# Optimization experiments

Hardware: AMD Instinct MI355X
Metric: run time of the kernel (lower is better)

Reference implementation:

```python
import jax, jax.numpy as jnp
import numpy as np

HIDDEN = 512
HEADS = 8
HEAD_DIM = HIDDEN // HEADS
THRESH = 0.1
EPS = 1e-8


def setup_inputs() -> dict:
    key = jax.random.key(0)
    ks = jax.random.split(key, 9)
    B, S = 2, 4096
    scale = 1.0 / np.sqrt(HIDDEN)
    x = jax.random.normal(ks[0], (B, S, HIDDEN), dtype=jnp.float32)
    Wq = jax.random.normal(ks[1], (HIDDEN, HIDDEN), dtype=jnp.float32) * scale
    bq = jnp.zeros((HIDDEN,), dtype=jnp.float32)
    Wk = jax.random.normal(ks[2], (HIDDEN, HIDDEN), dtype=jnp.float32) * scale
    bk = jnp.zeros((HIDDEN,), dtype=jnp.float32)
    Wv = jax.random.normal(ks[3], (HIDDEN, HIDDEN), dtype=jnp.float32) * scale
    bv = jnp.zeros((HIDDEN,), dtype=jnp.float32)
    Wo = jax.random.normal(ks[4], (HIDDEN, HIDDEN), dtype=jnp.float32) * scale
    bo = jnp.zeros((HIDDEN,), dtype=jnp.float32)
    return {"x": x, "Wq": Wq, "bq": bq, "Wk": Wk, "bk": bk,
            "Wv": Wv, "bv": bv, "Wo": Wo, "bo": bo}


def reference(x, Wq, bq, Wk, bk, Wv, bv, Wo, bo):
    B, S, _ = x.shape
    # torch Linear: y = x @ W.T + b
    def proj(W, b):
        y = jnp.einsum('bsd,ed->bse', x, W) + b
        return y.reshape(B, S, HEADS, HEAD_DIM).transpose(0, 2, 1, 3)  # [B,H,S,Dh]
    Q = proj(Wq, bq)
    K = proj(Wk, bk)
    V = proj(Wv, bv)
    scores = jnp.einsum('bhqd,bhkd->bhqk', Q, K) / jnp.sqrt(jnp.float32(HEAD_DIM))
    probs = jax.nn.softmax(scores, axis=-1)  # [B,H,S,S]
    probs = jnp.where(probs > THRESH, probs, 0.0)
    probs = probs / (jnp.sum(probs, axis=-1, keepdims=True) + EPS)
    ctx = jnp.einsum('bhqk,bhkd->bhqd', probs, V)
    ctx = ctx.transpose(0, 2, 1, 3).reshape(B, S, HIDDEN)
    return jnp.einsum('bsd,ed->bse', ctx, Wo) + bo
```

## Files before the change

kernel.cpp:

```cpp
#include <hip/hip_runtime.h>

#define S_LEN 4096
#define BATCH 2
#define HID 512
#define HEADS 8
#define HD 64
#define NX (BATCH * S_LEN * HID)
#define WSZ (HID * HID)
#define NBH (BATCH * HEADS)
#define QB 32
#define NB1 (S_LEN / QB * NBH)
#define NB2 (S_LEN / 64 * NBH)

typedef short v8s __attribute__((ext_vector_type(8)));
typedef float v4f __attribute__((ext_vector_type(4)));
typedef float v16f __attribute__((ext_vector_type(16)));
typedef unsigned short ushort_t;
typedef const __attribute__((address_space(1))) unsigned gu32;
typedef __attribute__((address_space(3))) unsigned lu32;

__device__ __forceinline__ ushort_t f2bf(float f) {
  unsigned u = __builtin_bit_cast(unsigned, f);
  u += 0x7fffu + ((u >> 16) & 1u);
  return (ushort_t)(u >> 16);
}
__device__ __forceinline__ unsigned pk2(float a, float b) {
  return (__builtin_bit_cast(unsigned, a) >> 16) |
         (__builtin_bit_cast(unsigned, b) & 0xFFFF0000u);
}
__device__ __forceinline__ float fexp2(float x) {
  return __builtin_amdgcn_exp2f(x);
}


__global__ __launch_bounds__(256) void cvt_k(
    const float* __restrict__ x,
    const float* __restrict__ wq, const float* __restrict__ wk,
    const float* __restrict__ wv, const float* __restrict__ wo,
    ushort_t* __restrict__ dst)
{
  const size_t e = ((size_t)blockIdx.x * 256 + threadIdx.x) * 4;
  const float* src; size_t off;
  if (e < NX) { src = x; off = e; }
  else {
    const size_t we = e - NX;
    const int wi = (int)(we >> 18);
    src = wi == 0 ? wq : wi == 1 ? wk : wi == 2 ? wv : wo;
    off = we & (WSZ - 1);
  }
  float4 v = *(const float4*)&src[off];
  uint2 u; u.x = pk2(v.x, v.y); u.y = pk2(v.z, v.w);
  *(uint2*)&dst[e] = u;
}

__global__ __launch_bounds__(256) void gemm_qkv(
    const ushort_t* __restrict__ X, const ushort_t* __restrict__ Wb,
    const float* __restrict__ bq, const float* __restrict__ bk, const float* __restrict__ bv,
    ushort_t* __restrict__ Qf, ushort_t* __restrict__ Kf, ushort_t* __restrict__ Vw,
    float qscale)
{
  __shared__ ushort_t As[128][32];
  __shared__ ushort_t Bs[128][32];
  const int t = threadIdx.x;
  const int lane = t & 63;
  const int l15 = lane & 15, lg = lane >> 4;
  const int w = t >> 6;
  const int wr = w >> 1, wc = w & 1;
  const int m0 = blockIdx.y * 128;
  const int wsel = blockIdx.x >> 2;
  const int e0 = (blockIdx.x & 3) * 128;
  const ushort_t* W = Wb + (size_t)wsel * WSZ;
  const float* bias = wsel == 0 ? bq : wsel == 1 ? bk : bv;
  const float osc = (wsel == 0) ? qscale : 1.0f;

  v4f acc[4][4] = {};
  const int r0 = t >> 2, c0 = (t & 3) * 8;

  for (int k0 = 0; k0 < HID; k0 += 32) {
    __syncthreads();
    __builtin_amdgcn_global_load_lds(
        (gu32*)(const void*)&X[(size_t)(m0 + r0) * HID + k0 + c0],
        (lu32*)(void*)&As[r0][c0], 16, 0, 0);
    __builtin_amdgcn_global_load_lds(
        (gu32*)(const void*)&X[(size_t)(m0 + r0 + 64) * HID + k0 + c0],
        (lu32*)(void*)&As[r0 + 64][c0], 16, 0, 0);
    __builtin_amdgcn_global_load_lds(
        (gu32*)(const void*)&W[(size_t)(e0 + r0) * HID + k0 + c0],
        (lu32*)(void*)&Bs[r0][c0], 16, 0, 0);
    __builtin_amdgcn_global_load_lds(
        (gu32*)(const void*)&W[(size_t)(e0 + r0 + 64) * HID + k0 + c0],
        (lu32*)(void*)&Bs[r0 + 64][c0], 16, 0, 0);
    __syncthreads();
    v8s a[4], b[4];
    #pragma unroll
    for (int fr = 0; fr < 4; ++fr)
      a[fr] = *(const v8s*)&As[wr * 64 + 16 * fr + l15][8 * lg];
    #pragma unroll
    for (int fc = 0; fc < 4; ++fc)
      b[fc] = *(const v8s*)&Bs[wc * 64 + 16 * fc + l15][8 * lg];
    #pragma unroll
    for (int fr = 0; fr < 4; ++fr)
      #pragma unroll
      for (int fc = 0; fc < 4; ++fc)
        acc[fr][fc] = __builtin_amdgcn_mfma_f32_16x16x32_bf16(a[fr], b[fc], acc[fr][fc], 0, 0, 0);
  }

  #pragma unroll
  for (int fr = 0; fr < 4; ++fr)
    #pragma unroll
    for (int fc = 0; fc < 4; ++fc) {
      const int e = e0 + wc * 64 + 16 * fc + l15;
      const float bval = bias[e];
      #pragma unroll
      for (int r = 0; r < 4; ++r) {
        const int m = m0 + wr * 64 + 16 * fr + 4 * lg + r;
        const float v = (acc[fr][fc][r] + bval) * osc;
        const int bidx = m >> 12, s = m & (S_LEN - 1);
        const int hh = e >> 6, dh = e & 63;
        const size_t hb = ((size_t)(bidx * HEADS + hh)) * (size_t)(S_LEN * HD);
        if (wsel == 2) {
          Vw[hb + (size_t)s * HD + dh] = f2bf(v);
        } else {
          const size_t off = (size_t)(s >> 5) * 2048 +
              (size_t)(((dh >> 4) * 64 + ((dh >> 3) & 1) * 32 + (s & 31)) * 8 + (dh & 7));
          (wsel == 0 ? Qf : Kf)[hb + off] = f2bf(v);
        }
      }
    }
}

__global__ __launch_bounds__(256, 4) void attn_p1(
    const ushort_t* __restrict__ Qf, const ushort_t* __restrict__ Kf,
    int* __restrict__ Flg)
{
  __shared__ float RedL[4][QB];
  __shared__ float RedM[4][QB];
  __shared__ int bflag;
  const int t = threadIdx.x;
  const int lane = t & 63;
  const int l31 = lane & 31, hi = lane >> 5;
  const int kq = t >> 6;
  const int lin = blockIdx.x;
  const int bh = ((lin & 7) << 1) | ((lin >> 3) & 1);
  const int q0 = (lin >> 4) * QB;
  if (t == 0) bflag = 0;

  const size_t hoff = (size_t)bh * (size_t)(S_LEN * HD);
  const ushort_t* Qb = Qf + hoff + (size_t)(q0 >> 5) * 2048;
  const ushort_t* Kb = Kf + hoff;

  v8s qa[4];
  #pragma unroll
  for (int ks = 0; ks < 4; ++ks)
    qa[ks] = *(const v8s*)&Qb[(ks * 64 + lane) * 8];

  float M[16], L[16];
  #pragma unroll
  for (int j = 0; j < 16; ++j) { M[j] = -1e30f; L[j] = 0.f; }

  v8s kA[4], kB4[4];
  {
    const ushort_t* kc = Kb + (size_t)kq * 2048;
    #pragma unroll
    for (int ks = 0; ks < 4; ++ks)
      kA[ks] = *(const v8s*)&kc[(ks * 64 + lane) * 8];
  }

#define PROC(KX)                                                            \
  {                                                                         \
    v16f s = {};                                                            \
    _Pragma("unroll")                                                       \
    for (int ks = 0; ks < 4; ++ks)                                          \
      s = __builtin_amdgcn_mfma_f32_32x32x16_bf16(qa[ks], KX[ks], s, 0, 0, 0); \
    _Pragma("unroll")                                                       \
    for (int j = 0; j < 16; ++j) {                                          \
      M[j] = fmaxf(M[j], s[j]);                                             \
      L[j] += fexp2(s[j]);                                                  \
    }                                                                       \
  }

  for (int i = 0; i < 32; i += 2) {
    {
      const ushort_t* kc = Kb + (size_t)(kq + 4 * (i + 1)) * 2048;
      #pragma unroll
      for (int ks = 0; ks < 4; ++ks)
        kB4[ks] = *(const v8s*)&kc[(ks * 64 + lane) * 8];
    }
    PROC(kA)
    {
      const int c2 = (i + 2 < 32) ? (kq + 4 * (i + 2)) : kq;
      const ushort_t* kc = Kb + (size_t)c2 * 2048;
      #pragma unroll
      for (int ks = 0; ks < 4; ++ks)
        kA[ks] = *(const v8s*)&kc[(ks * 64 + lane) * 8];
    }
    PROC(kB4)
  }
#undef PROC

  #pragma unroll
  for (int j = 0; j < 16; ++j) {
    float Lv = L[j], Mv = M[j];
    Lv += __shfl_xor(Lv, 1);  Mv = fmaxf(Mv, __shfl_xor(Mv, 1));
    Lv += __shfl_xor(Lv, 2);  Mv = fmaxf(Mv, __shfl_xor(Mv, 2));
    Lv += __shfl_xor(Lv, 4);  Mv = fmaxf(Mv, __shfl_xor(Mv, 4));
    Lv += __shfl_xor(Lv, 8);  Mv = fmaxf(Mv, __shfl_xor(Mv, 8));
    Lv += __shfl_xor(Lv, 16); Mv = fmaxf(Mv, __shfl_xor(Mv, 16));
    if (l31 == 0) {
      const int row = (j & 3) + 8 * (j >> 2) + 4 * hi;
      RedL[kq][row] = Lv;
      RedM[kq][row] = Mv;
    }
  }
  __syncthreads();
  if (t < QB) {
    const float Lv = RedL[0][t] + RedL[1][t] + RedL[2][t] + RedL[3][t];
    const float Mv = fmaxf(fmaxf(RedM[0][t], RedM[1][t]),
                           fmaxf(RedM[2][t], RedM[3][t]));
    if (Mv >= __log2f(Lv) - 3.3719281f) atomicOr(&bflag, 1);
  }
  __syncthreads();
  if (t == 0) Flg[lin] = bflag;
}

__global__ __launch_bounds__(256) void attn_p2(
    const ushort_t* __restrict__ Qf, const ushort_t* __restrict__ Kf,
    const ushort_t* __restrict__ V, ushort_t* __restrict__ Cb,
    const int* __restrict__ Flg)
{
  const int lin = blockIdx.x;
  {
    const int base = lin & 15, qb = lin >> 4;
    if ((Flg[base | ((2 * qb) << 4)] | Flg[base | ((2 * qb + 1) << 4)]) == 0)
      return;
  }
  __shared__ float Osh[64][HD + 1];
  __shared__ float Dsh[64];
  __shared__ float RedA[4][64];
  __shared__ float iLs[64];
  __shared__ ushort_t Pp[4][32][40];
  __shared__ ushort_t VT[4][HD][40];
  const int t = threadIdx.x;
  const int lane = t & 63;
  const int l31 = lane & 31, hi = lane >> 5;
  const int w = t >> 6;
  const int bh = ((lin & 7) << 1) | ((lin >> 3) & 1);
  const int q0 = (lin >> 4) * 64;
  const size_t hoff = (size_t)bh * (size_t)(S_LEN * HD);
  const ushort_t* Qb = Qf + hoff + (size_t)(q0 >> 5) * 2048;
  const ushort_t* Kb = Kf + hoff;
  const ushort_t* Vh = V + hoff;

  if (t < 64) Dsh[t] = 0.f;
  for (int idx = t; idx < 64 * HD; idx += 256) Osh[idx >> 6][idx & 63] = 0.f;

  v8s qa[4], qB[4];
  #pragma unroll
  for (int ks = 0; ks < 4; ++ks) {
    qa[ks] = *(const v8s*)&Qb[(ks * 64 + lane) * 8];
    qB[ks] = *(const v8s*)&Qb[2048 + (ks * 64 + lane) * 8];
  }

  float L0[16], L1[16];
  #pragma unroll
  for (int j = 0; j < 16; ++j) { L0[j] = 0.f; L1[j] = 0.f; }
  for (int i = 0; i < 32; ++i) {
    const ushort_t* kc = Kb + (size_t)(w + 4 * i) * 2048;
    v8s kb[4];
    #pragma unroll
    for (int ks = 0; ks < 4; ++ks)
      kb[ks] = *(const v8s*)&kc[(ks * 64 + lane) * 8];
    v16f sa = {}, sb = {};
    #pragma unroll
    for (int ks = 0; ks < 4; ++ks) {
      sa = __builtin_amdgcn_mfma_f32_32x32x16_bf16(qa[ks], kb[ks], sa, 0, 0, 0);
      sb = __builtin_amdgcn_mfma_f32_32x32x16_bf16(qB[ks], kb[ks], sb, 0, 0, 0);
    }
    #pragma unroll
    for (int j = 0; j < 16; ++j) {
      L0[j] += fexp2(sa[j]);
      L1[j] += fexp2(sb[j]);
    }
  }
  #pragma unroll
  for (int rseti = 0; rseti < 2; ++rseti)
    #pragma unroll
    for (int j = 0; j < 16; ++j) {
      float Lv = (rseti == 0) ? L0[j] : L1[j];
      Lv += __shfl_xor(Lv, 1);  Lv += __shfl_xor(Lv, 2);
      Lv += __shfl_xor(Lv, 4);  Lv += __shfl_xor(Lv, 8);
      Lv += __shfl_xor(Lv, 16);
      if (l31 == 0) {
        const int row = rseti * 32 + (j & 3) + 8 * (j >> 2) + 4 * hi;
        RedA[w][row] = Lv;
      }
    }
  __syncthreads();
  if (t < 64)
    iLs[t] = 1.0f / (RedA[0][t] + RedA[1][t] + RedA[2][t] + RedA[3][t]);
  __syncthreads();

  float il[2][16];
  #pragma unroll
  for (int rseti = 0; rseti < 2; ++rseti)
    #pragma unroll
    for (int j = 0; j < 16; ++j)
      il[rseti][j] = iLs[rseti * 32 + (j & 3) + 8 * (j >> 2) + 4 * hi];

  v16f oA[2] = {}, oB[2] = {};
  float den[2][16] = {};

  for (int i = 0; i < 32; ++i) {
    const int c = w + 4 * i;
    const ushort_t* kc = Kb + (size_t)c * 2048;
    v8s kb[4];
    #pragma unroll
    for (int ks = 0; ks < 4; ++ks)
      kb[ks] = *(const v8s*)&kc[(ks * 64 + lane) * 8];
    v16f sa = {}, sb = {};
    #pragma unroll
    for (int ks = 0; ks < 4; ++ks) {
      sa = __builtin_amdgcn_mfma_f32_32x32x16_bf16(qa[ks], kb[ks], sa, 0, 0, 0);
      sb = __builtin_amdgcn_mfma_f32_32x32x16_bf16(qB[ks], kb[ks], sb, 0, 0, 0);
    }
    {
      const ushort_t* vsrc = &Vh[((size_t)c * 32 + l31) * HD + hi * 32];
      #pragma unroll
      for (int qq = 0; qq < 4; ++qq) {
        uint4 vv = *(const uint4*)&vsrc[qq * 8];
        const ushort_t* pv = (const ushort_t*)&vv;
        #pragma unroll
        for (int jj = 0; jj < 8; ++jj)
          VT[w][hi * 32 + qq * 8 + jj][l31] = pv[jj];
      }
    }
    #pragma unroll
    for (int rseti = 0; rseti < 2; ++rseti) {
      #pragma unroll
      for (int j = 0; j < 16; ++j) {
        const float s = (rseti == 0) ? sa[j] : sb[j];
        const int row = (j & 3) + 8 * (j >> 2) + 4 * hi;
        float p = fexp2(s) * il[rseti][j];
        p = (p > 0.1f) ? p : 0.f;
        den[rseti][j] += p;
        Pp[w][row][l31] = f2bf(p);
      }
      v8s pa0 = *(const v8s*)&Pp[w][l31][8 * hi];
      v8s pa1 = *(const v8s*)&Pp[w][l31][16 + 8 * hi];
      #pragma unroll
      for (int dblk = 0; dblk < 2; ++dblk) {
        v8s vb0 = *(const v8s*)&VT[w][dblk * 32 + l31][8 * hi];
        v8s vb1 = *(const v8s*)&VT[w][dblk * 32 + l31][16 + 8 * hi];
        if (rseti == 0) {
          oA[dblk] = __builtin_amdgcn_mfma_f32_32x32x16_bf16(pa0, vb0, oA[dblk], 0, 0, 0);
          oA[dblk] = __builtin_amdgcn_mfma_f32_32x32x16_bf16(pa1, vb1, oA[dblk], 0, 0, 0);
        } else {
          oB[dblk] = __builtin_amdgcn_mfma_f32_32x32x16_bf16(pa0, vb0, oB[dblk], 0, 0, 0);
          oB[dblk] = __builtin_amdgcn_mfma_f32_32x32x16_bf16(pa1, vb1, oB[dblk], 0, 0, 0);
        }
      }
    }
  }

  #pragma unroll
  for (int rseti = 0; rseti < 2; ++rseti)
    #pragma unroll
    for (int j = 0; j < 16; ++j) {
      float d = den[rseti][j];
      d += __shfl_xor(d, 1); d += __shfl_xor(d, 2); d += __shfl_xor(d, 4);
      d += __shfl_xor(d, 8); d += __shfl_xor(d, 16);
      const int row = rseti * 32 + (j & 3) + 8 * (j >> 2) + 4 * hi;
      if (l31 == 0) atomicAdd(&Dsh[row], d);
    }
  #pragma unroll
  for (int rseti = 0; rseti < 2; ++rseti)
    #pragma unroll
    for (int dblk = 0; dblk < 2; ++dblk)
      #pragma unroll
      for (int j = 0; j < 16; ++j) {
        const int row = rseti * 32 + (j & 3) + 8 * (j >> 2) + 4 * hi;
        const float val = (rseti == 0) ? oA[dblk][j] : oB[dblk][j];
        atomicAdd(&Osh[row][dblk * 32 + l31], val);
      }
  __syncthreads();
  const int b = bh >> 3, h = bh & 7;
  for (int idx = t; idx < 64 * HD; idx += 256) {
    const int row = idx >> 6, d = idx & 63;
    const float val = Osh[row][d] / (Dsh[row] + 1e-8f);
    Cb[((size_t)b * S_LEN + q0 + row) * HID + h * HD + d] = f2bf(val);
  }
}

__global__ __launch_bounds__(256) void gemm_out(
    const ushort_t* __restrict__ X, const ushort_t* __restrict__ W,
    const float* __restrict__ bias, const int* __restrict__ Flg,
    float* __restrict__ Df)
{
  const int t = threadIdx.x;
  const int m0 = blockIdx.y * 64;
  const int e0 = blockIdx.x * 64;

  int fm = 0;
  {
    const int b = m0 >> 12, qblk = (m0 & (S_LEN - 1)) >> 6;
    #pragma unroll
    for (int h = 0; h < HEADS; ++h) {
      const int bhh = b * HEADS + h;
      const int base = (bhh >> 1) | ((bhh & 1) << 3);
      const int f = Flg[base | ((2 * qblk) << 4)] |
                    Flg[base | ((2 * qblk + 1) << 4)];
      fm |= (f ? 1 : 0) << h;
    }
    if (!fm) {
      const int row = t >> 2, c0 = (t & 3) * 16;
      #pragma unroll
      for (int g = 0; g < 4; ++g) {
        const float4 bv = *(const float4*)&bias[e0 + c0 + g * 4];
        *(float4*)&Df[(size_t)(m0 + row) * HID + e0 + c0 + g * 4] = bv;
      }
      return;
    }
  }

  __shared__ ushort_t As[64][40];
  __shared__ ushort_t Bs[64][40];
  const int lane = t & 63;
  const int l15 = lane & 15, lg = lane >> 4;
  const int w = t >> 6;
  const int wr = w >> 1, wc = w & 1;

  v4f acc[2][2] = {};
  const int srow = t >> 2, scol = (t & 3) * 8;
  const uint4 zu = {0u, 0u, 0u, 0u};

  for (int k0 = 0; k0 < HID; k0 += 32) {
    __syncthreads();
    const bool hot = (fm >> (k0 >> 6)) & 1;
    *(uint4*)&As[srow][scol] = hot
        ? *(const uint4*)&X[(size_t)(m0 + srow) * HID + k0 + scol]
        : zu;
    *(uint4*)&Bs[srow][scol] =
        *(const uint4*)&W[(size_t)(e0 + srow) * HID + k0 + scol];
    __syncthreads();
    v8s a[2], b[2];
    #pragma unroll
    for (int fr = 0; fr < 2; ++fr)
      a[fr] = *(const v8s*)&As[wr * 32 + 16 * fr + l15][8 * lg];
    #pragma unroll
    for (int fc = 0; fc < 2; ++fc)
      b[fc] = *(const v8s*)&Bs[wc * 32 + 16 * fc + l15][8 * lg];
    #pragma unroll
    for (int fr = 0; fr < 2; ++fr)
      #pragma unroll
      for (int fc = 0; fc < 2; ++fc)
        acc[fr][fc] = __builtin_amdgcn_mfma_f32_16x16x32_bf16(a[fr], b[fc], acc[fr][fc], 0, 0, 0);
  }

  #pragma unroll
  for (int fr = 0; fr < 2; ++fr)
    #pragma unroll
    for (int fc = 0; fc < 2; ++fc) {
      const int e = e0 + wc * 32 + 16 * fc + l15;
      const float bval = bias[e];
      #pragma unroll
      for (int r = 0; r < 4; ++r) {
        const int m = m0 + wr * 32 + 16 * fr + 4 * lg + r;
        Df[(size_t)m * HID + e] = acc[fr][fc][r] + bval;
      }
    }
}

extern "C" void kernel_launch(void* const* d_in, const int* in_sizes, int n_in,
                              void* d_out, int out_size, void* d_ws, size_t ws_size,
                              hipStream_t stream) {
  const float* x  = (const float*)d_in[0];
  const float* Wq = (const float*)d_in[1];
  const float* bq = (const float*)d_in[2];
  const float* Wk = (const float*)d_in[3];
  const float* bk = (const float*)d_in[4];
  const float* Wv = (const float*)d_in[5];
  const float* bv = (const float*)d_in[6];
  const float* Wo = (const float*)d_in[7];
  const float* bo = (const float*)d_in[8];

  int*      Flg  = (int*)d_ws;
  ushort_t* xb   = (ushort_t*)(Flg + NB1);
  ushort_t* wqb  = xb + NX;
  ushort_t* wob  = wqb + 3 * WSZ;
  ushort_t* Qf   = wob + WSZ;
  ushort_t* Kf   = Qf + NX;
  ushort_t* Vw   = Kf + NX;
  ushort_t* Cb   = Vw + NX;

  const float qscale = 0.125f * 1.44269504f;

  cvt_k<<<(NX + 4 * WSZ) / 1024, 256, 0, stream>>>(x, Wq, Wk, Wv, Wo, xb);

  gemm_qkv<<<dim3(12, 64), 256, 0, stream>>>(
      xb, wqb, bq, bk, bv, Qf, Kf, Vw, qscale);

  attn_p1<<<NB1, 256, 0, stream>>>(Qf, Kf, Flg);
  attn_p2<<<NB2, 256, 0, stream>>>(Qf, Kf, Vw, Cb, Flg);

  gemm_out<<<dim3(8, 128), 256, 0, stream>>>(Cb, wob, bo, Flg, (float*)d_out);
}
```

Before: 103.9 us.

## Replace exp-based block screening with cheap max-minus-mean pre-filter plus refinement pass

The first attention pass no longer evaluates exp2 on every score. It accumulates the row max and the row sum of scores, then flags a 64-row block only when max minus mean exceeds a fixed margin, since only such rows can hold a probability above the threshold. A new refinement kernel reruns the exact max-versus-log-sum-exp test, but only on flagged blocks, and the main pass and output GEMM read the refined flags at 64-row granularity. This removes the transcendental work from the screening pass at the cost of one extra kernel launch and recomputing QK^T for flagged blocks. Correctness depends on the max-minus-mean bound being conservative.

```diff
diff --git a/kernel.cpp b/kernel.cpp
--- a/kernel.cpp
+++ b/kernel.cpp
@@ -8,9 +8,8 @@
 #define NX (BATCH * S_LEN * HID)
 #define WSZ (HID * HID)
 #define NBH (BATCH * HEADS)
-#define QB 32
-#define NB1 (S_LEN / QB * NBH)
-#define NB2 (S_LEN / 64 * NBH)
+#define QB 64
+#define NBLK (S_LEN / QB * NBH)
 
 typedef short v8s __attribute__((ext_vector_type(8)));
 typedef float v4f __attribute__((ext_vector_type(4)));
@@ -129,24 +128,26 @@
     }
 }
 
-__global__ __launch_bounds__(256, 4) void attn_p1(
+__global__ __launch_bounds__(512, 4) void attn_p1(
     const ushort_t* __restrict__ Qf, const ushort_t* __restrict__ Kf,
-    int* __restrict__ Flg)
+    int* __restrict__ JFlg)
 {
-  __shared__ float RedL[4][QB];
+  __shared__ float RedS[4][QB];
   __shared__ float RedM[4][QB];
   __shared__ int bflag;
   const int t = threadIdx.x;
   const int lane = t & 63;
   const int l31 = lane & 31, hi = lane >> 5;
-  const int kq = t >> 6;
+  const int w = t >> 6;
+  const int rs = w >> 2;
+  const int kq = w & 3;
   const int lin = blockIdx.x;
   const int bh = ((lin & 7) << 1) | ((lin >> 3) & 1);
   const int q0 = (lin >> 4) * QB;
   if (t == 0) bflag = 0;
 
   const size_t hoff = (size_t)bh * (size_t)(S_LEN * HD);
-  const ushort_t* Qb = Qf + hoff + (size_t)(q0 >> 5) * 2048;
+  const ushort_t* Qb = Qf + hoff + ((size_t)(q0 >> 5) + rs) * 2048;
   const ushort_t* Kb = Kf + hoff;
 
   v8s qa[4];
@@ -154,9 +155,9 @@
   for (int ks = 0; ks < 4; ++ks)
     qa[ks] = *(const v8s*)&Qb[(ks * 64 + lane) * 8];
 
-  float M[16], L[16];
-  #pragma unroll
-  for (int j = 0; j < 16; ++j) { M[j] = -1e30f; L[j] = 0.f; }
+  float M[16], S[16];
+  #pragma unroll
+  for (int j = 0; j < 16; ++j) { M[j] = -1e30f; S[j] = 0.f; }
 
   v8s kA[4], kB4[4];
   {
@@ -175,7 +176,7 @@
     _Pragma("unroll")                                                       \
     for (int j = 0; j < 16; ++j) {                                          \
       M[j] = fmaxf(M[j], s[j]);                                             \
-      L[j] += fexp2(s[j]);                                                  \
+      S[j] += s[j];                                                         \
     }                                                                       \
   }
 
@@ -200,18 +201,105 @@
 
   #pragma unroll
   for (int j = 0; j < 16; ++j) {
-    float Lv = L[j], Mv = M[j];
-    Lv += __shfl_xor(Lv, 1);  Mv = fmaxf(Mv, __shfl_xor(Mv, 1));
-    Lv += __shfl_xor(Lv, 2);  Mv = fmaxf(Mv, __shfl_xor(Mv, 2));
-    Lv += __shfl_xor(Lv, 4);  Mv = fmaxf(Mv, __shfl_xor(Mv, 4));
-    Lv += __shfl_xor(Lv, 8);  Mv = fmaxf(Mv, __shfl_xor(Mv, 8));
-    Lv += __shfl_xor(Lv, 16); Mv = fmaxf(Mv, __shfl_xor(Mv, 16));
+    float Sv = S[j], Mv = M[j];
+    Sv += __shfl_xor(Sv, 1);  Mv = fmaxf(Mv, __shfl_xor(Mv, 1));
+    Sv += __shfl_xor(Sv, 2);  Mv = fmaxf(Mv, __shfl_xor(Mv, 2));
+    Sv += __shfl_xor(Sv, 4);  Mv = fmaxf(Mv, __shfl_xor(Mv, 4));
+    Sv += __shfl_xor(Sv, 8);  Mv = fmaxf(Mv, __shfl_xor(Mv, 8));
+    Sv += __shfl_xor(Sv, 16); Mv = fmaxf(Mv, __shfl_xor(Mv, 16));
     if (l31 == 0) {
-      const int row = (j & 3) + 8 * (j >> 2) + 4 * hi;
-      RedL[kq][row] = Lv;
+      const int row = rs * 32 + (j & 3) + 8 * (j >> 2) + 4 * hi;
+      RedS[kq][row] = Sv;
       RedM[kq][row] = Mv;
     }
   }
+  __syncthreads();
+  if (t < QB) {
+    const float Sv = RedS[0][t] + RedS[1][t] + RedS[2][t] + RedS[3][t];
+    const float Mv = fmaxf(fmaxf(RedM[0][t], RedM[1][t]),
+                           fmaxf(RedM[2][t], RedM[3][t]));
+    if (Mv - Sv * (1.0f / 4096.0f) > 8.3f) atomicOr(&bflag, 1);
+  }
+  __syncthreads();
+  if (t == 0) JFlg[lin] = bflag;
+}
+
+__global__ __launch_bounds__(256) void attn_ref(
+    const ushort_t* __restrict__ Qf, const ushort_t* __restrict__ Kf,
+    const int* __restrict__ JFlg, int* __restrict__ RFlg)
+{
+  const int lin = blockIdx.x;
+  if (JFlg[lin] == 0) { if (threadIdx.x == 0) RFlg[lin] = 0; return; }
+  __shared__ float RedL[4][QB];
+  __shared__ float RedM[4][QB];
+  __shared__ int bflag;
+  const int t = threadIdx.x;
+  const int lane = t & 63;
+  const int l31 = lane & 31, hi = lane >> 5;
+  const int w = t >> 6;
+  const int bh = ((lin & 7) << 1) | ((lin >> 3) & 1);
+  const int q0 = (lin >> 4) * QB;
+  if (t == 0) bflag = 0;
+
+  const size_t hoff = (size_t)bh * (size_t)(S_LEN * HD);
+  const ushort_t* Qb = Qf + hoff + (size_t)(q0 >> 5) * 2048;
+  const ushort_t* Kb = Kf + hoff;
+
+  v8s qa[4], qB[4];
+  #pragma unroll
+  for (int ks = 0; ks < 4; ++ks) {
+    qa[ks] = *(const v8s*)&Qb[(ks * 64 + lane) * 8];
+    qB[ks] = *(const v8s*)&Qb[2048 + (ks * 64 + lane) * 8];
+  }
+
+  float L0[16], L1[16], M0[16], M1[16];
+  #pragma unroll
+  for (int j = 0; j < 16; ++j) {
+    L0[j] = 0.f; L1[j] = 0.f; M0[j] = -1e30f; M1[j] = -1e30f;
+  }
+
+  for (int i = 0; i < 32; ++i) {
+    const ushort_t* kc = Kb + (size_t)(w + 4 * i) * 2048;
+    v8s kb[4];
+    #pragma unroll
+    for (int ks = 0; ks < 4; ++ks)
+      kb[ks] = *(const v8s*)&kc[(ks * 64 + lane) * 8];
+    v16f sa = {}, sb = {};
+    #pragma unroll
+    for (int ks = 0; ks < 4; ++ks)
+      sa = __builtin_amdgcn_mfma_f32_32x32x16_bf16(qa[ks], kb[ks], sa, 0, 0, 0);
+    #pragma unroll
+    for (int ks = 0; ks < 4; ++ks)
+      sb = __builtin_amdgcn_mfma_f32_32x32x16_bf16(qB[ks], kb[ks], sb, 0, 0, 0);
+    #pragma unroll
+    for (int j = 0; j < 16; ++j) {
+      M0[j] = fmaxf(M0[j], sa[j]);
+      L0[j] += fexp2(sa[j]);
+    }
+    #pragma unroll
+    for (int j = 0; j < 16; ++j) {
+      M1[j] = fmaxf(M1[j], sb[j]);
+      L1[j] += fexp2(sb[j]);
+    }
+  }
+
+  #pragma unroll
+  for (int rseti = 0; rseti < 2; ++rseti)
+    #pragma unroll
+    for (int j = 0; j < 16; ++j) {
+      float Lv = (rseti == 0) ? L0[j] : L1[j];
+      float Mv = (rseti == 0) ? M0[j] : M1[j];
+      Lv += __shfl_xor(Lv, 1);  Mv = fmaxf(Mv, __shfl_xor(Mv, 1));
+      Lv += __shfl_xor(Lv, 2);  Mv = fmaxf(Mv, __shfl_xor(Mv, 2));
+      Lv += __shfl_xor(Lv, 4);  Mv = fmaxf(Mv, __shfl_xor(Mv, 4));
+      Lv += __shfl_xor(Lv, 8);  Mv = fmaxf(Mv, __shfl_xor(Mv, 8));
+      Lv += __shfl_xor(Lv, 16); Mv = fmaxf(Mv, __shfl_xor(Mv, 16));
+      if (l31 == 0) {
+        const int row = rseti * 32 + (j & 3) + 8 * (j >> 2) + 4 * hi;
+        RedL[w][row] = Lv;
+        RedM[w][row] = Mv;
+      }
+    }
   __syncthreads();
   if (t < QB) {
     const float Lv = RedL[0][t] + RedL[1][t] + RedL[2][t] + RedL[3][t];
@@ -220,24 +308,20 @@
     if (Mv >= __log2f(Lv) - 3.3719281f) atomicOr(&bflag, 1);
   }
   __syncthreads();
-  if (t == 0) Flg[lin] = bflag;
+  if (t == 0) RFlg[lin] = bflag;
 }
 
 __global__ __launch_bounds__(256) void attn_p2(
     const ushort_t* __restrict__ Qf, const ushort_t* __restrict__ Kf,
     const ushort_t* __restrict__ V, ushort_t* __restrict__ Cb,
-    const int* __restrict__ Flg)
+    const int* __restrict__ RFlg)
 {
   const int lin = blockIdx.x;
-  {
-    const int base = lin & 15, qb = lin >> 4;
-    if ((Flg[base | ((2 * qb) << 4)] | Flg[base | ((2 * qb + 1) << 4)]) == 0)
-      return;
-  }
-  __shared__ float Osh[64][HD + 1];
-  __shared__ float Dsh[64];
-  __shared__ float RedA[4][64];
-  __shared__ float iLs[64];
+  if (RFlg[lin] == 0) return;
+  __shared__ float Osh[QB][HD + 1];
+  __shared__ float Dsh[QB];
+  __shared__ float RedA[4][QB];
+  __shared__ float iLs[QB];
   __shared__ ushort_t Pp[4][32][40];
   __shared__ ushort_t VT[4][HD][40];
   const int t = threadIdx.x;
@@ -245,14 +329,14 @@
   const int l31 = lane & 31, hi = lane >> 5;
   const int w = t >> 6;
   const int bh = ((lin & 7) << 1) | ((lin >> 3) & 1);
-  const int q0 = (lin >> 4) * 64;
+  const int q0 = (lin >> 4) * QB;
   const size_t hoff = (size_t)bh * (size_t)(S_LEN * HD);
   const ushort_t* Qb = Qf + hoff + (size_t)(q0 >> 5) * 2048;
   const ushort_t* Kb = Kf + hoff;
   const ushort_t* Vh = V + hoff;
 
-  if (t < 64) Dsh[t] = 0.f;
-  for (int idx = t; idx < 64 * HD; idx += 256) Osh[idx >> 6][idx & 63] = 0.f;
+  if (t < QB) Dsh[t] = 0.f;
+  for (int idx = t; idx < QB * HD; idx += 256) Osh[idx >> 6][idx & 63] = 0.f;
 
   v8s qa[4], qB[4];
   #pragma unroll
@@ -296,7 +380,7 @@
       }
     }
   __syncthreads();
-  if (t < 64)
+  if (t < QB)
     iLs[t] = 1.0f / (RedA[0][t] + RedA[1][t] + RedA[2][t] + RedA[3][t]);
   __syncthreads();
 
@@ -384,7 +468,7 @@
       }
   __syncthreads();
   const int b = bh >> 3, h = bh & 7;
-  for (int idx = t; idx < 64 * HD; idx += 256) {
+  for (int idx = t; idx < QB * HD; idx += 256) {
     const int row = idx >> 6, d = idx & 63;
     const float val = Osh[row][d] / (Dsh[row] + 1e-8f);
     Cb[((size_t)b * S_LEN + q0 + row) * HID + h * HD + d] = f2bf(val);
@@ -393,7 +477,7 @@
 
 __global__ __launch_bounds__(256) void gemm_out(
     const ushort_t* __restrict__ X, const ushort_t* __restrict__ W,
-    const float* __restrict__ bias, const int* __restrict__ Flg,
+    const float* __restrict__ bias, const int* __restrict__ RFlg,
     float* __restrict__ Df)
 {
   const int t = threadIdx.x;
@@ -407,9 +491,7 @@
     for (int h = 0; h < HEADS; ++h) {
       const int bhh = b * HEADS + h;
       const int base = (bhh >> 1) | ((bhh & 1) << 3);
-      const int f = Flg[base | ((2 * qblk) << 4)] |
-                    Flg[base | ((2 * qblk + 1) << 4)];
-      fm |= (f ? 1 : 0) << h;
+      fm |= (RFlg[base | (qblk << 4)] ? 1 : 0) << h;
     }
     if (!fm) {
       const int row = t >> 2, c0 = (t & 3) * 16;
@@ -483,8 +565,9 @@
   const float* Wo = (const float*)d_in[7];
   const float* bo = (const float*)d_in[8];
 
-  int*      Flg  = (int*)d_ws;
-  ushort_t* xb   = (ushort_t*)(Flg + NB1);
+  int*      JFlg = (int*)d_ws;
+  int*      RFlg = JFlg + NBLK;
+  ushort_t* xb   = (ushort_t*)(RFlg + NBLK);
   ushort_t* wqb  = xb + NX;
   ushort_t* wob  = wqb + 3 * WSZ;
   ushort_t* Qf   = wob + WSZ;
@@ -499,8 +582,9 @@
   gemm_qkv<<<dim3(12, 64), 256, 0, stream>>>(
       xb, wqb, bq, bk, bv, Qf, Kf, Vw, qscale);
 
-  attn_p1<<<NB1, 256, 0, stream>>>(Qf, Kf, Flg);
-  attn_p2<<<NB2, 256, 0, stream>>>(Qf, Kf, Vw, Cb, Flg);
-
-  gemm_out<<<dim3(8, 128), 256, 0, stream>>>(Cb, wob, bo, Flg, (float*)d_out);
-}
+  attn_p1<<<NBLK, 512, 0, stream>>>(Qf, Kf, JFlg);
+  attn_ref<<<NBLK, 256, 0, stream>>>(Qf, Kf, JFlg, RFlg);
+  attn_p2<<<NBLK, 256, 0, stream>>>(Qf, Kf, Vw, Cb, RFlg);
+
+  gemm_out<<<dim3(8, 128), 256, 0, stream>>>(Cb, wob, bo, RFlg, (float*)d_out);
+}
```

New measurement: 128.4 us. +23.6%, slower.
